# Kernel tuning notes

Measured on AMD Instinct MI355X. Metric: run time of the kernel, lower is better.

The kernel has to match this reference:

```python
import jax, jax.numpy as jnp
import numpy as np

B, S, C = 2, 2048, 1024          # batch, seq (= text_max_block_size), channels
H, D = 16, 64                    # num_heads, key_dim (C // H)
TEMP = 1e4                       # RoPE temperature
NEG_INF = -1e9


def rope(x):
    # x: [B, S, H, D]; interleaved-pair rotary embedding over sequence positions
    b, s, h, d = x.shape
    half = d // 2
    dim_t = TEMP ** (jnp.arange(half, dtype=jnp.float32) / half)      # [half]
    ang = jnp.arange(s, dtype=jnp.float32)[:, None] / dim_t            # [S, half]
    sin = jnp.sin(ang)[None, :, None, :]                               # [1,S,1,half]
    cos = jnp.cos(ang)[None, :, None, :]
    xr = x.reshape(b, s, h, half, 2)
    x1, x2 = xr[..., 0], xr[..., 1]
    out = jnp.stack([x1 * cos - x2 * sin, x2 * cos + x1 * sin], axis=-1)
    return out.reshape(b, s, h, d)


def setup_inputs() -> dict:
    key = jax.random.key(0)
    ks = jax.random.split(key, 5)
    w_scale = 0.02
    return {
        "x": jax.random.normal(ks[0], (B, S, C), jnp.float32),
        "w_qkv": jax.random.normal(ks[1], (C, 3 * C), jnp.float32) * w_scale,
        "q_bias": jax.random.normal(ks[2], (C,), jnp.float32) * w_scale,
        "v_bias": jax.random.normal(ks[3], (C,), jnp.float32) * w_scale,
        "w_out": jax.random.normal(ks[4], (C, C), jnp.float32) * w_scale,
    }


def reference(x, w_qkv, q_bias, v_bias, w_out):
    # fused QKV projection (no bias: qkv_bias=False)
    qkv = x @ w_qkv                                   # [B,S,3C]
    q, k, v = jnp.split(qkv, 3, axis=-1)
    # qv_bias=True: learnable bias on query and value only
    q = q + q_bias
    v = v + v_bias
    # inline RoPE on Q/K (PositionalEncodingFourierRot1D on [.., H, D/2, 2])
    q = rope(q.reshape(B, S, H, D))                   # [B,S,H,D]
    k = rope(k.reshape(B, S, H, D))
    v = v.reshape(B, S, H, D)
    scale = 1.0 / jnp.sqrt(jnp.float32(D))            # qk_scale <= 0 -> 1/sqrt(key_dim)
    scores = jnp.einsum("bqhd,bkhd->bhqk", q, k) * scale
    # CausalMask injected between scores and softmax
    causal = jnp.tril(jnp.ones((S, S), dtype=bool))
    scores = jnp.where(causal[None, None], scores, jnp.float32(NEG_INF))
    attn = jax.nn.softmax(scores, axis=-1)
    out = jnp.einsum("bhqk,bkhd->bqhd", attn, v).reshape(B, S, C)
    # output projection (return_weight=True, return_bias=False)
    return out @ w_out
```

## Files before the change

### kernel.cpp

```cpp
#include <hip/hip_runtime.h>
#include <stdint.h>

#define AS1 __attribute__((address_space(1)))
#define AS3 __attribute__((address_space(3)))

typedef __attribute__((ext_vector_type(8))) short bf16x8;
typedef __attribute__((ext_vector_type(4))) float f32x4;

__device__ __forceinline__ unsigned short f32_bf16(float f) {
  __bf16 b = (__bf16)f;
  union { __bf16 b; unsigned short u; } cv;
  cv.b = b;
  return cv.u;
}

__device__ __forceinline__ void async_ld16(const unsigned short* g, unsigned short* l) {
  __builtin_amdgcn_global_load_lds((const AS1 void*)g, (AS3 void*)l, 16, 0, 0);
}

__device__ __forceinline__ void transpose_tile(const float* __restrict__ src,
                                               unsigned short* __restrict__ dst,
                                               int K, int N, int nt, int kt,
                                               unsigned short (*tile)[65]) {
  int t = threadIdx.x;
  #pragma unroll
  for (int i = 0; i < 16; ++i) {
    int idx = t + i * 256;
    int r = idx >> 6, c = idx & 63;
    tile[r][c] = f32_bf16(src[(size_t)(kt * 64 + r) * N + nt * 64 + c]);
  }
  __syncthreads();
  #pragma unroll
  for (int i = 0; i < 16; ++i) {
    int idx = t + i * 256;
    int r = idx >> 6, c = idx & 63;
    dst[(size_t)(nt * 64 + r) * K + kt * 64 + c] = tile[c][r];
  }
}

__global__ __launch_bounds__(256) void prep(const float* __restrict__ x,
                                            const float* __restrict__ w_qkv,
                                            const float* __restrict__ w_out,
                                            unsigned short* __restrict__ Xb,
                                            unsigned short* __restrict__ WqkvT,
                                            unsigned short* __restrict__ WoT,
                                            float2* __restrict__ ropeT) {
  __shared__ unsigned short tile[64][65];
  int bid = blockIdx.x;
  if (bid < 4096) {
    int i = bid * 256 + threadIdx.x;
    float4 v = ((const float4*)x)[i];
    ushort4 o;
    o.x = f32_bf16(v.x); o.y = f32_bf16(v.y); o.z = f32_bf16(v.z); o.w = f32_bf16(v.w);
    ((ushort4*)Xb)[i] = o;
  } else if (bid < 4864) {
    int b2 = bid - 4096;
    transpose_tile(w_qkv, WqkvT, 1024, 3072, b2 % 48, b2 / 48, tile);
  } else if (bid < 5120) {
    int b2 = bid - 4864;
    transpose_tile(w_out, WoT, 1024, 1024, b2 % 16, b2 / 16, tile);
  } else {
    int idx = (bid - 5120) * 256 + threadIdx.x;
    int s = idx >> 5, p = idx & 31;
    float invf = exp2f((float)p * (-13.287712379549449f / 32.f));
    float sn, cs;
    __sincosf((float)s * invf, &sn, &cs);
    ropeT[idx] = make_float2(cs, sn);
  }
}

template <int KDIM>
__device__ __forceinline__ void gemm_core_k64(const unsigned short* __restrict__ A,
                                              const unsigned short* __restrict__ Bt,
                                              unsigned short* Als, unsigned short* Bls,
                                              int bm, int bn, f32x4 (&acc)[4][4]) {
  const int tid = threadIdx.x;
  const int w = tid >> 6, lane = tid & 63, quad = lane >> 4, l15 = lane & 15;
  const int wr = w >> 1, wc = w & 1;
  const int srow = lane >> 2, scol = (lane & 3) * 8;
  const unsigned short* Arow0 = A + (size_t)(bm * 128) * KDIM;
  const unsigned short* Brow0 = Bt + (size_t)(bn * 128) * KDIM;
  for (int k0 = 0; k0 < KDIM; k0 += 64) {
    __syncthreads();
    #pragma unroll
    for (int i = 0; i < 4; ++i) {
      int row = (i & 1) * 64 + w * 16 + srow;
      int kadd = (i >> 1) * 32 + scol;
      async_ld16(Arow0 + (size_t)row * KDIM + k0 + kadd, Als + i * 2048 + w * 512 + lane * 8);
      async_ld16(Brow0 + (size_t)row * KDIM + k0 + kadd, Bls + i * 2048 + w * 512 + lane * 8);
    }
    __syncthreads();
    #pragma unroll
    for (int kk2 = 0; kk2 < 2; ++kk2) {
      bf16x8 a[4], b[4];
      #pragma unroll
      for (int mi = 0; mi < 4; ++mi)
        a[mi] = *(const bf16x8*)(Als + kk2 * 4096 + (wr * 64 + mi * 16 + l15) * 32 + quad * 8);
      #pragma unroll
      for (int ni = 0; ni < 4; ++ni)
        b[ni] = *(const bf16x8*)(Bls + kk2 * 4096 + (wc * 64 + ni * 16 + l15) * 32 + quad * 8);
      #pragma unroll
      for (int mi = 0; mi < 4; ++mi)
        #pragma unroll
        for (int ni = 0; ni < 4; ++ni)
          acc[mi][ni] = __builtin_amdgcn_mfma_f32_16x16x32_bf16(a[mi], b[ni], acc[mi][ni], 0, 0, 0);
    }
  }
}

__global__ __launch_bounds__(256, 4) void qkv_gemm(const unsigned short* __restrict__ Xb,
                                                   const unsigned short* __restrict__ WqkvT,
                                                   const float* __restrict__ qbias,
                                                   const float* __restrict__ vbias,
                                                   const float2* __restrict__ ropeT,
                                                   unsigned short* __restrict__ Qg,
                                                   unsigned short* __restrict__ Kg,
                                                   unsigned short* __restrict__ Vtg) {
  __shared__ unsigned short shm[4 * 64 * 72];
  unsigned short* Als = shm;
  unsigned short* Bls = shm + 8192;
  f32x4 acc[4][4] = {};
  const int bn = blockIdx.x, bm = blockIdx.y;
  gemm_core_k64<1024>(Xb, WqkvT, Als, Bls, bm, bn, acc);
  __syncthreads();

  const int tid = threadIdx.x;
  const int w = tid >> 6, lane = tid & 63, quad = lane >> 4, l15 = lane & 15;
  const int wr = w >> 1, wc = w & 1;
  const int part = bn >> 3;
  const int cb = (bn & 7) * 128 + wc * 64;
  const int h = cb >> 6;
  const int m0 = bm * 128 + wr * 64;
  const int bb = m0 >> 11, s0 = m0 & 2047;
  unsigned short* Sw = shm + w * 4608;

  if (part < 2) {
    const float qscale = (part == 0) ? 0.18033688011112042f : 1.f;
    #pragma unroll
    for (int ni = 0; ni < 4; ++ni) {
      int dd = ni * 16 + l15;
      float bias = (part == 0) ? qbias[cb + dd] : 0.f;
      float sgn = (dd & 1) ? 1.f : -1.f;
      const float2* tp = ropeT + (size_t)s0 * 32 + (dd >> 1);
      #pragma unroll
      for (int mi = 0; mi < 4; ++mi) {
        #pragma unroll
        for (int r = 0; r < 4; ++r) {
          int sl = mi * 16 + quad * 4 + r;
          float val = acc[mi][ni][r] + bias;
          float partner = __shfl_xor(val, 1);
          float2 cssn = tp[sl * 32];
          val = (val * cssn.x + sgn * partner * cssn.y) * qscale;
          Sw[sl * 72 + dd] = f32_bf16(val);
        }
      }
    }
    unsigned short* dstp = (part == 0) ? Qg : Kg;
    const size_t base = ((size_t)(bb * 16 + h) * 2048 + s0) * 64;
    #pragma unroll
    for (int it = 0; it < 8; ++it) {
      int row = it * 8 + (lane >> 3), off = (lane & 7) * 8;
      bf16x8 v = *(const bf16x8*)(Sw + row * 72 + off);
      *(bf16x8*)(dstp + base + (size_t)row * 64 + off) = v;
    }
  } else {
    #pragma unroll
    for (int ni = 0; ni < 4; ++ni) {
      int dd = ni * 16 + l15;
      float bias = vbias[cb + dd];
      #pragma unroll
      for (int mi = 0; mi < 4; ++mi)
        #pragma unroll
        for (int r = 0; r < 4; ++r) {
          int sl = mi * 16 + quad * 4 + r;
          Sw[sl * 68 + dd] = f32_bf16(acc[mi][ni][r] + bias);
        }
    }
    const size_t vbase = (size_t)(bb * 16 + h) * 64 * 2048 + s0;
    #pragma unroll 4
    for (int dd = 0; dd < 64; ++dd) {
      unsigned short v = Sw[lane * 68 + dd];
      Vtg[vbase + (size_t)dd * 2048 + lane] = v;
    }
  }
}

__global__ __launch_bounds__(256, 4) void attn_fwd(const unsigned short* __restrict__ Qg,
                                                   const unsigned short* __restrict__ Kg,
                                                   const unsigned short* __restrict__ Vtg,
                                                   unsigned short* __restrict__ Og) {
  __shared__ unsigned short Kls[2][64 * 64];
  __shared__ unsigned short Vls[2][64 * 64];
  __shared__ unsigned short Pls[4][16 * 64];
  const int bid = blockIdx.x;
  const int ix = bid >> 3;
  const int bh = ((bid & 7) << 2) + (ix & 3);
  const int s = ix >> 2;
  const int m = s & 7, t = s >> 3;
  const int qt = (t == 0) ? m : (t == 1) ? (31 - m) : (t == 2) ? (8 + m) : (23 - m);
  const int h = bh & 15, b = bh >> 4;
  const int tid = threadIdx.x;
  const int w = tid >> 6, lane = tid & 63, quad = lane >> 4, l15 = lane & 15;
  const unsigned short* Qb = Qg + (size_t)bh * 2048 * 64;
  const unsigned short* Kb = Kg + (size_t)bh * 2048 * 64;
  const unsigned short* Vb = Vtg + (size_t)bh * 64 * 2048;
  const int q0 = qt * 64 + w * 16;

  bf16x8 aq[2];
  #pragma unroll
  for (int ki = 0; ki < 2; ++ki)
    aq[ki] = *(const bf16x8*)(Qb + (size_t)(q0 + l15) * 64 + ki * 32 + quad * 8);

  f32x4 o[4] = {};
  float l_st[4] = {0.f, 0.f, 0.f, 0.f};

  unsigned short* Pw = Pls[w];
  const int nkt = qt + 1;

  const int srow = tid >> 2, scol = (tid & 3) * 8;

  #pragma unroll
  for (int i = 0; i < 2; ++i) {
    async_ld16(Kb + (size_t)srow * 64 + i * 32 + scol, Kls[0] + i * 2048 + tid * 8);
    async_ld16(Vb + (size_t)srow * 2048 + i * 32 + scol, Vls[0] + i * 2048 + tid * 8);
  }

  for (int kt = 0; kt < nkt; ++kt) {
    __syncthreads();
    const int cur = kt & 1;
    if (kt + 1 < nkt) {
      const int nxt = cur ^ 1;
      #pragma unroll
      for (int i = 0; i < 2; ++i) {
        async_ld16(Kb + (size_t)((kt + 1) * 64 + srow) * 64 + i * 32 + scol,
                   Kls[nxt] + i * 2048 + tid * 8);
        async_ld16(Vb + (size_t)srow * 2048 + (kt + 1) * 64 + i * 32 + scol,
                   Vls[nxt] + i * 2048 + tid * 8);
      }
    }
    const unsigned short* Kbuf = Kls[cur];
    const unsigned short* Vbuf = Vls[cur];

    f32x4 sc[4] = {};
    #pragma unroll
    for (int ki = 0; ki < 2; ++ki) {
      bf16x8 bk[4];
      #pragma unroll
      for (int ni = 0; ni < 4; ++ni)
        bk[ni] = *(const bf16x8*)(Kbuf + ki * 2048 + (ni * 16 + l15) * 32 + quad * 8);
      #pragma unroll
      for (int ni = 0; ni < 4; ++ni)
        sc[ni] = __builtin_amdgcn_mfma_f32_16x16x32_bf16(aq[ki], bk[ni], sc[ni], 0, 0, 0);
    }

    if (kt == qt) {
      #pragma unroll
      for (int r = 0; r < 4; ++r) {
        int row = q0 + quad * 4 + r;
        #pragma unroll
        for (int ni = 0; ni < 4; ++ni) {
          bool masked = (kt * 64 + ni * 16 + l15) > row;
          float pv = __builtin_amdgcn_exp2f(sc[ni][r] - 8.f);
          pv = masked ? 0.f : pv;
          sc[ni][r] = pv;
          l_st[r] += pv;
        }
      }
    } else {
      #pragma unroll
      for (int r = 0; r < 4; ++r)
        #pragma unroll
        for (int ni = 0; ni < 4; ++ni) {
          float pv = __builtin_amdgcn_exp2f(sc[ni][r] - 8.f);
          sc[ni][r] = pv;
          l_st[r] += pv;
        }
    }

    #pragma unroll
    for (int nl = 0; nl < 4; ++nl) {
      int ck = ((nl & 1) << 1) | (l15 >> 3);
      int cs = ck ^ quad;
      #pragma unroll
      for (int r = 0; r < 4; ++r) {
        int rw = quad * 4 + r;
        Pw[(nl >> 1) * 512 + rw * 32 + cs * 8 + (l15 & 7)] = f32_bf16(sc[nl][r]);
      }
    }
    #pragma unroll
    for (int k4 = 0; k4 < 2; ++k4) {
      bf16x8 ap, bv[4];
      int csr = quad ^ ((l15 >> 2) & 3);
      ap = *(const bf16x8*)(Pw + k4 * 512 + l15 * 32 + csr * 8);
      #pragma unroll
      for (int di = 0; di < 4; ++di)
        bv[di] = *(const bf16x8*)(Vbuf + k4 * 2048 + (di * 16 + l15) * 32 + quad * 8);
      #pragma unroll
      for (int di = 0; di < 4; ++di)
        o[di] = __builtin_amdgcn_mfma_f32_16x16x32_bf16(ap, bv[di], o[di], 0, 0, 0);
    }
  }

  #pragma unroll
  for (int r = 0; r < 4; ++r) {
    float s2 = l_st[r];
    s2 += __shfl_xor(s2, 1);
    s2 += __shfl_xor(s2, 2);
    s2 += __shfl_xor(s2, 4);
    s2 += __shfl_xor(s2, 8);
    l_st[r] = 1.f / s2;
  }
  #pragma unroll
  for (int r = 0; r < 4; ++r) {
    float inv = l_st[r];
    int sl = quad * 4 + r;
    #pragma unroll
    for (int di = 0; di < 4; ++di) {
      int ck = di * 2 + (l15 >> 3);
      int cs = ck ^ (sl & 7);
      Pw[sl * 64 + cs * 8 + (l15 & 7)] = f32_bf16(o[di][r] * inv);
    }
  }
  const size_t ob = ((size_t)(b * 2048 + q0)) * 1024 + h * 64;
  #pragma unroll
  for (int it = 0; it < 2; ++it) {
    int row = it * 8 + (lane >> 3);
    int cs = (lane & 7) ^ (row & 7);
    bf16x8 v = *(const bf16x8*)(Pw + row * 64 + cs * 8);
    *(bf16x8*)(Og + ob + (size_t)row * 1024 + (lane & 7) * 8) = v;
  }
}

__global__ __launch_bounds__(256, 4) void out_gemm(const unsigned short* __restrict__ Og,
                                                   const unsigned short* __restrict__ WoT,
                                                   float* __restrict__ Cout) {
  __shared__ unsigned short Als[2 * 64 * 32];
  __shared__ unsigned short Bls[2 * 128 * 32];
  f32x4 acc[4][2] = {};
  const int bn = blockIdx.x, bm = blockIdx.y;
  const int tid = threadIdx.x;
  const int w = tid >> 6, lane = tid & 63, quad = lane >> 4, l15 = lane & 15;
  const int srow = lane >> 2, scol = (lane & 3) * 8;
  const unsigned short* Arow0 = Og + (size_t)(bm * 64) * 1024;
  const unsigned short* Brow0 = WoT + (size_t)(bn * 128) * 1024;
  for (int k0 = 0; k0 < 1024; k0 += 64) {
    __syncthreads();
    #pragma unroll
    for (int i = 0; i < 2; ++i) {
      int arow = w * 16 + srow;
      async_ld16(Arow0 + (size_t)arow * 1024 + k0 + i * 32 + scol,
                 Als + i * 2048 + w * 512 + lane * 8);
    }
    #pragma unroll
    for (int i = 0; i < 4; ++i) {
      int brow = (i & 1) * 64 + w * 16 + srow;
      int kadd = (i >> 1) * 32 + scol;
      async_ld16(Brow0 + (size_t)brow * 1024 + k0 + kadd,
                 Bls + i * 2048 + w * 512 + lane * 8);
    }
    __syncthreads();
    #pragma unroll
    for (int kk2 = 0; kk2 < 2; ++kk2) {
      bf16x8 a[4], b[2];
      #pragma unroll
      for (int mi = 0; mi < 4; ++mi)
        a[mi] = *(const bf16x8*)(Als + kk2 * 2048 + (mi * 16 + l15) * 32 + quad * 8);
      #pragma unroll
      for (int ni = 0; ni < 2; ++ni)
        b[ni] = *(const bf16x8*)(Bls + kk2 * 4096 + (w * 32 + ni * 16 + l15) * 32 + quad * 8);
      #pragma unroll
      for (int mi = 0; mi < 4; ++mi)
        #pragma unroll
        for (int ni = 0; ni < 2; ++ni)
          acc[mi][ni] = __builtin_amdgcn_mfma_f32_16x16x32_bf16(a[mi], b[ni], acc[mi][ni], 0, 0, 0);
    }
  }
  #pragma unroll
  for (int mi = 0; mi < 4; ++mi)
    #pragma unroll
    for (int r = 0; r < 4; ++r) {
      int mm = bm * 64 + mi * 16 + quad * 4 + r;
      #pragma unroll
      for (int ni = 0; ni < 2; ++ni) {
        int n = bn * 128 + w * 32 + ni * 16 + l15;
        Cout[(size_t)mm * 1024 + n] = acc[mi][ni][r];
      }
    }
}

extern "C" void kernel_launch(void* const* d_in, const int* in_sizes, int n_in,
                              void* d_out, int out_size, void* d_ws, size_t ws_size,
                              hipStream_t stream) {
  const float* x      = (const float*)d_in[0];
  const float* w_qkv  = (const float*)d_in[1];
  const float* q_bias = (const float*)d_in[2];
  const float* v_bias = (const float*)d_in[3];
  const float* w_out  = (const float*)d_in[4];
  float* out = (float*)d_out;

  char* ws = (char*)d_ws;
  unsigned short* Xb    = (unsigned short*)(ws);
  unsigned short* WqkvT = (unsigned short*)(ws + (8u  << 20));
  unsigned short* WoT   = (unsigned short*)(ws + (14u << 20));
  unsigned short* Qg    = (unsigned short*)(ws + (16u << 20));
  unsigned short* Kg    = (unsigned short*)(ws + (24u << 20));
  unsigned short* Vtg   = (unsigned short*)(ws + (32u << 20));
  unsigned short* Og    = (unsigned short*)(ws + (40u << 20));
  float2* ropeT         = (float2*)(ws + (48u << 20));

  prep<<<5376, 256, 0, stream>>>(x, w_qkv, w_out, Xb, WqkvT, WoT, ropeT);
  qkv_gemm<<<dim3(24, 32), 256, 0, stream>>>(Xb, WqkvT, q_bias, v_bias, ropeT, Qg, Kg, Vtg);
  attn_fwd<<<1024, 256, 0, stream>>>(Qg, Kg, Vtg, Og);
  out_gemm<<<dim3(8, 64), 256, 0, stream>>>(Og, WoT, out);
}
```

Measured before the change: 176.9 us.

## Switch attention to 32x32 MFMA tiles with 128-row query blocks

```diff
diff --git a/kernel.cpp b/kernel.cpp
--- a/kernel.cpp
+++ b/kernel.cpp
@@ -6,6 +6,7 @@
 
 typedef __attribute__((ext_vector_type(8))) short bf16x8;
 typedef __attribute__((ext_vector_type(4))) float f32x4;
+typedef __attribute__((ext_vector_type(16))) float f32x16;
 
 __device__ __forceinline__ unsigned short f32_bf16(float f) {
   __bf16 b = (__bf16)f;
@@ -185,37 +186,39 @@
   }
 }
 
-__global__ __launch_bounds__(256, 4) void attn_fwd(const unsigned short* __restrict__ Qg,
+__global__ __launch_bounds__(256, 2) void attn_fwd(const unsigned short* __restrict__ Qg,
                                                    const unsigned short* __restrict__ Kg,
                                                    const unsigned short* __restrict__ Vtg,
                                                    unsigned short* __restrict__ Og) {
-  __shared__ unsigned short Kls[2][64 * 64];
-  __shared__ unsigned short Vls[2][64 * 64];
-  __shared__ unsigned short Pls[4][16 * 64];
+  __shared__ unsigned short Kls[2][2 * 64 * 32];
+  __shared__ unsigned short Vls[2][2 * 64 * 32];
+  __shared__ unsigned short Pls[4][32 * 32];
   const int bid = blockIdx.x;
   const int ix = bid >> 3;
   const int bh = ((bid & 7) << 2) + (ix & 3);
   const int s = ix >> 2;
-  const int m = s & 7, t = s >> 3;
-  const int qt = (t == 0) ? m : (t == 1) ? (31 - m) : (t == 2) ? (8 + m) : (23 - m);
+  const int qt = (s < 8) ? s : 23 - s;
   const int h = bh & 15, b = bh >> 4;
   const int tid = threadIdx.x;
-  const int w = tid >> 6, lane = tid & 63, quad = lane >> 4, l15 = lane & 15;
+  const int w = tid >> 6, lane = tid & 63;
+  const int r32 = lane & 31, hi = lane >> 5;
   const unsigned short* Qb = Qg + (size_t)bh * 2048 * 64;
   const unsigned short* Kb = Kg + (size_t)bh * 2048 * 64;
   const unsigned short* Vb = Vtg + (size_t)bh * 64 * 2048;
-  const int q0 = qt * 64 + w * 16;
-
-  bf16x8 aq[2];
-  #pragma unroll
-  for (int ki = 0; ki < 2; ++ki)
-    aq[ki] = *(const bf16x8*)(Qb + (size_t)(q0 + l15) * 64 + ki * 32 + quad * 8);
-
-  f32x4 o[4] = {};
-  float l_st[4] = {0.f, 0.f, 0.f, 0.f};
+  const int q0 = qt * 128 + w * 32;
+
+  bf16x8 aq[4];
+  #pragma unroll
+  for (int kk = 0; kk < 4; ++kk)
+    aq[kk] = *(const bf16x8*)(Qb + (size_t)(q0 + r32) * 64 + kk * 16 + hi * 8);
+
+  f32x16 o0 = {}, o1 = {};
+  float l_st[16];
+  #pragma unroll
+  for (int r = 0; r < 16; ++r) l_st[r] = 0.f;
 
   unsigned short* Pw = Pls[w];
-  const int nkt = qt + 1;
+  const int nkt = 2 * qt + 2;
 
   const int srow = tid >> 2, scol = (tid & 3) * 8;
 
@@ -241,93 +244,64 @@
     const unsigned short* Kbuf = Kls[cur];
     const unsigned short* Vbuf = Vls[cur];
 
-    f32x4 sc[4] = {};
-    #pragma unroll
-    for (int ki = 0; ki < 2; ++ki) {
-      bf16x8 bk[4];
-      #pragma unroll
-      for (int ni = 0; ni < 4; ++ni)
-        bk[ni] = *(const bf16x8*)(Kbuf + ki * 2048 + (ni * 16 + l15) * 32 + quad * 8);
-      #pragma unroll
-      for (int ni = 0; ni < 4; ++ni)
-        sc[ni] = __builtin_amdgcn_mfma_f32_16x16x32_bf16(aq[ki], bk[ni], sc[ni], 0, 0, 0);
-    }
-
-    if (kt == qt) {
-      #pragma unroll
-      for (int r = 0; r < 4; ++r) {
-        int row = q0 + quad * 4 + r;
-        #pragma unroll
-        for (int ni = 0; ni < 4; ++ni) {
-          bool masked = (kt * 64 + ni * 16 + l15) > row;
-          float pv = __builtin_amdgcn_exp2f(sc[ni][r] - 8.f);
-          pv = masked ? 0.f : pv;
-          sc[ni][r] = pv;
+    #pragma unroll
+    for (int kc = 0; kc < 2; ++kc) {
+      f32x16 sc = {};
+      #pragma unroll
+      for (int kk = 0; kk < 4; ++kk) {
+        bf16x8 bk = *(const bf16x8*)(Kbuf + (kk >> 1) * 2048 + (kc * 32 + r32) * 32 +
+                                     (kk & 1) * 16 + hi * 8);
+        sc = __builtin_amdgcn_mfma_f32_32x32x16_bf16(aq[kk], bk, sc, 0, 0, 0);
+      }
+
+      if (kt >= 2 * qt) {
+        int key = kt * 64 + kc * 32 + r32;
+        #pragma unroll
+        for (int r = 0; r < 16; ++r) {
+          int rowl = (r & 3) + 8 * (r >> 2) + 4 * hi;
+          float pv = __builtin_amdgcn_exp2f(sc[r] - 8.f);
+          pv = (key > q0 + rowl) ? 0.f : pv;
           l_st[r] += pv;
+          Pw[rowl * 32 + r32] = f32_bf16(pv);
         }
-      }
-    } else {
-      #pragma unroll
-      for (int r = 0; r < 4; ++r)
-        #pragma unroll
-        for (int ni = 0; ni < 4; ++ni) {
-          float pv = __builtin_amdgcn_exp2f(sc[ni][r] - 8.f);
-          sc[ni][r] = pv;
+      } else {
+        #pragma unroll
+        for (int r = 0; r < 16; ++r) {
+          int rowl = (r & 3) + 8 * (r >> 2) + 4 * hi;
+          float pv = __builtin_amdgcn_exp2f(sc[r] - 8.f);
           l_st[r] += pv;
+          Pw[rowl * 32 + r32] = f32_bf16(pv);
         }
-    }
-
-    #pragma unroll
-    for (int nl = 0; nl < 4; ++nl) {
-      int ck = ((nl & 1) << 1) | (l15 >> 3);
-      int cs = ck ^ quad;
-      #pragma unroll
-      for (int r = 0; r < 4; ++r) {
-        int rw = quad * 4 + r;
-        Pw[(nl >> 1) * 512 + rw * 32 + cs * 8 + (l15 & 7)] = f32_bf16(sc[nl][r]);
-      }
-    }
-    #pragma unroll
-    for (int k4 = 0; k4 < 2; ++k4) {
-      bf16x8 ap, bv[4];
-      int csr = quad ^ ((l15 >> 2) & 3);
-      ap = *(const bf16x8*)(Pw + k4 * 512 + l15 * 32 + csr * 8);
-      #pragma unroll
-      for (int di = 0; di < 4; ++di)
-        bv[di] = *(const bf16x8*)(Vbuf + k4 * 2048 + (di * 16 + l15) * 32 + quad * 8);
-      #pragma unroll
-      for (int di = 0; di < 4; ++di)
-        o[di] = __builtin_amdgcn_mfma_f32_16x16x32_bf16(ap, bv[di], o[di], 0, 0, 0);
-    }
-  }
-
-  #pragma unroll
-  for (int r = 0; r < 4; ++r) {
+      }
+
+      #pragma unroll
+      for (int ks = 0; ks < 2; ++ks) {
+        bf16x8 ap  = *(const bf16x8*)(Pw + r32 * 32 + ks * 16 + hi * 8);
+        bf16x8 bv0 = *(const bf16x8*)(Vbuf + kc * 2048 + (r32) * 32 + ks * 16 + hi * 8);
+        bf16x8 bv1 = *(const bf16x8*)(Vbuf + kc * 2048 + (32 + r32) * 32 + ks * 16 + hi * 8);
+        o0 = __builtin_amdgcn_mfma_f32_32x32x16_bf16(ap, bv0, o0, 0, 0, 0);
+        o1 = __builtin_amdgcn_mfma_f32_32x32x16_bf16(ap, bv1, o1, 0, 0, 0);
+      }
+    }
+  }
+
+  #pragma unroll
+  for (int r = 0; r < 16; ++r) {
     float s2 = l_st[r];
     s2 += __shfl_xor(s2, 1);
     s2 += __shfl_xor(s2, 2);
     s2 += __shfl_xor(s2, 4);
     s2 += __shfl_xor(s2, 8);
+    s2 += __shfl_xor(s2, 16);
     l_st[r] = 1.f / s2;
   }
-  #pragma unroll
-  for (int r = 0; r < 4; ++r) {
-    float inv = l_st[r];
-    int sl = quad * 4 + r;
-    #pragma unroll
-    for (int di = 0; di < 4; ++di) {
-      int ck = di * 2 + (l15 >> 3);
-      int cs = ck ^ (sl & 7);
-      Pw[sl * 64 + cs * 8 + (l15 & 7)] = f32_bf16(o[di][r] * inv);
-    }
-  }
-  const size_t ob = ((size_t)(b * 2048 + q0)) * 1024 + h * 64;
-  #pragma unroll
-  for (int it = 0; it < 2; ++it) {
-    int row = it * 8 + (lane >> 3);
-    int cs = (lane & 7) ^ (row & 7);
-    bf16x8 v = *(const bf16x8*)(Pw + row * 64 + cs * 8);
-    *(bf16x8*)(Og + ob + (size_t)row * 1024 + (lane & 7) * 8) = v;
+  const size_t ob = ((size_t)b * 2048) * 1024 + (size_t)h * 64;
+  #pragma unroll
+  for (int r = 0; r < 16; ++r) {
+    int row = q0 + (r & 3) + 8 * (r >> 2) + 4 * hi;
+    size_t base = ob + (size_t)row * 1024;
+    Og[base + r32]      = f32_bf16(o0[r] * l_st[r]);
+    Og[base + 32 + r32] = f32_bf16(o1[r] * l_st[r]);
   }
 }
 
@@ -410,6 +384,6 @@
 
   prep<<<5376, 256, 0, stream>>>(x, w_qkv, w_out, Xb, WqkvT, WoT, ropeT);
   qkv_gemm<<<dim3(24, 32), 256, 0, stream>>>(Xb, WqkvT, q_bias, v_bias, ropeT, Qg, Kg, Vtg);
-  attn_fwd<<<1024, 256, 0, stream>>>(Qg, Kg, Vtg, Og);
+  attn_fwd<<<512, 256, 0, stream>>>(Qg, Kg, Vtg, Og);
   out_gemm<<<dim3(8, 64), 256, 0, stream>>>(Og, WoT, out);
 }
```

Result: slower. 193.2 us (+9.2%).
